# Optimization experiments

Measured on AMD Instinct MI355X. Metric: run time of the kernel, lower is better.

Reference implementation:

```python
import jax, jax.numpy as jnp
import numpy as np

V = 50000      # variables -> 2V literals
C = 200000     # clauses
E = 300000     # edges per polarity
EMB = 128
NFC = 3
ROUNDS = 26


def setup_inputs() -> dict:
    key = jax.random.key(0)
    ks = jax.random.split(key, 16)
    s = 0.05
    f32 = jnp.float32
    inp = {
        "l_pos_emb": jax.random.normal(ks[0], (V, EMB), f32) * s,
        "l_neg_emb": jax.random.normal(ks[1], (V, EMB), f32) * s,
        "c_emb": jax.random.normal(ks[2], (C, EMB), f32) * s,
        "l_mlp_W": jax.random.normal(ks[3], (NFC, EMB, EMB), f32) * s,
        "l_mlp_b": jnp.zeros((NFC, EMB), f32),
        "c_mlp_W": jax.random.normal(ks[4], (NFC, EMB, EMB), f32) * s,
        "c_mlp_b": jnp.zeros((NFC, EMB), f32),
        "l_Wih": jax.random.normal(ks[5], (4 * EMB, 2 * EMB), f32) * s,
        "l_Whh": jax.random.normal(ks[6], (4 * EMB, EMB), f32) * s,
        "l_bih": jnp.zeros((4 * EMB,), f32),
        "l_bhh": jnp.zeros((4 * EMB,), f32),
        "c_Wih": jax.random.normal(ks[7], (4 * EMB, EMB), f32) * s,
        "c_Whh": jax.random.normal(ks[8], (4 * EMB, EMB), f32) * s,
        "c_bih": jnp.zeros((4 * EMB,), f32),
        "c_bhh": jnp.zeros((4 * EMB,), f32),
        "pos_src": jax.random.randint(ks[9], (E,), 0, V, jnp.int32),
        "pos_dst": jax.random.randint(ks[10], (E,), 0, C, jnp.int32),
        "neg_src": jax.random.randint(ks[11], (E,), 0, V, jnp.int32),
        "neg_dst": jax.random.randint(ks[12], (E,), 0, C, jnp.int32),
    }
    return inp


def _mlp(x, W, b):
    # num_fc Linear layers with ReLU between (no final activation)
    n = W.shape[0]
    for i in range(n):
        x = x @ W[i] + b[i]
        if i < n - 1:
            x = jax.nn.relu(x)
    return x


def _lstm_cell(x, h, c, Wih, Whh, bih, bhh):
    # torch nn.LSTM single step; gate order i, f, g, o
    gates = x @ Wih.T + h @ Whh.T + bih + bhh
    i, f, g, o = jnp.split(gates, 4, axis=1)
    c_new = jax.nn.sigmoid(f) * c + jax.nn.sigmoid(i) * jnp.tanh(g)
    h_new = jax.nn.sigmoid(o) * jnp.tanh(c_new)
    return h_new, c_new


def reference(l_pos_emb, l_neg_emb, c_emb,
              l_mlp_W, l_mlp_b, c_mlp_W, c_mlp_b,
              l_Wih, l_Whh, l_bih, l_bhh,
              c_Wih, c_Whh, c_bih, c_bhh,
              pos_src, pos_dst, neg_src, neg_dst):
    num_v = l_pos_emb.shape[0]
    num_c = c_emb.shape[0]
    l_h = jnp.concatenate([l_pos_emb, l_neg_emb], axis=0)   # [2V, E]
    l_c = jnp.zeros_like(l_h)
    c_h = c_emb
    c_c = jnp.zeros_like(c_h)

    def round_fn(carry, _):
        l_h, l_c, c_h, c_c = carry
        # literal -> clause messages
        l_msg = _mlp(l_h, l_mlp_W, l_mlp_b)
        pos_msg, neg_msg = l_msg[:num_v], l_msg[num_v:]
        l2c = (jax.ops.segment_sum(pos_msg[pos_src], pos_dst, num_segments=num_c)
               + jax.ops.segment_sum(neg_msg[neg_src], neg_dst, num_segments=num_c))
        # clause -> literal messages (reverse edges)
        c_msg = _mlp(c_h, c_mlp_W, c_mlp_b)
        pos_c2l = jax.ops.segment_sum(c_msg[pos_dst], pos_src, num_segments=num_v)
        neg_c2l = jax.ops.segment_sum(c_msg[neg_dst], neg_src, num_segments=num_v)
        c2l = jnp.concatenate([pos_c2l, neg_c2l], axis=0)    # [2V, E]
        # flip literal hidden (pair each literal with its negation)
        flip = jnp.concatenate([l_h[num_v:], l_h[:num_v]], axis=0)
        l_x = jnp.concatenate([c2l, flip], axis=1)           # [2V, 2E]
        l_h, l_c = _lstm_cell(l_x, l_h, l_c, l_Wih, l_Whh, l_bih, l_bhh)
        c_h, c_c = _lstm_cell(l2c, c_h, c_c, c_Wih, c_Whh, c_bih, c_bhh)
        return (l_h, l_c, c_h, c_c), None

    (l_h, l_c, c_h, c_c), _ = jax.lax.scan(round_fn, (l_h, l_c, c_h, c_c),
                                           None, length=ROUNDS)
    # concat final literal and clause embeddings: [2V + C, EMB]
    return jnp.concatenate([l_h, c_h], axis=0)
```

## Files before the change

### kernel.cpp

```cpp
#include <hip/hip_runtime.h>
#include <math.h>

typedef __attribute__((ext_vector_type(8))) short short8;
typedef __attribute__((ext_vector_type(4))) float f32x4;
typedef unsigned short ushort_t;

constexpr int NV = 50000;
constexpr int NL = 100000;
constexpr int NC = 200000;
constexpr int NE = 300000;
constexpr int NROUNDS = 26;

__device__ __forceinline__ float sigf(float x) { return 1.0f / (1.0f + __expf(-x)); }

__device__ __forceinline__ void split1(float x, ushort_t* h, ushort_t* l) {
    unsigned u = __float_as_uint(x);
    *h = (ushort_t)(u >> 16);
    float lf = x - __uint_as_float(u & 0xffff0000u);
    *l = (ushort_t)(__float_as_uint(lf) >> 16);
}
__device__ __forceinline__ float recf(ushort_t h, ushort_t l) {
    return __uint_as_float((unsigned)h << 16) + __uint_as_float((unsigned)l << 16);
}

__device__ __forceinline__ void splitw(float x, ushort_t* h, ushort_t* l) {
    unsigned u = __float_as_uint(x);
    unsigned hr = (u + 0x7fffu + ((u >> 16) & 1u)) & 0xffff0000u;
    float lf = x - __uint_as_float(hr);
    unsigned ul = __float_as_uint(lf);
    *h = (ushort_t)(hr >> 16);
    *l = (ushort_t)((ul + 0x7fffu + ((ul >> 16) & 1u)) >> 16);
}


__global__ __launch_bounds__(256) void split_rows_k(
    const float* __restrict__ src, ushort_t* __restrict__ dst, int total)
{
    for (int i = blockIdx.x * 256 + threadIdx.x; i < total; i += gridDim.x * 256) {
        int row = i >> 7, c = i & 127;
        ushort_t h, l;
        split1(src[i], &h, &l);
        dst[(size_t)row * 256 + c] = h;
        dst[(size_t)row * 256 + 128 + c] = l;
    }
}

__global__ __launch_bounds__(256) void convert_out_k(
    const ushort_t* __restrict__ src, float* __restrict__ dst, int total)
{
    for (int i = blockIdx.x * 256 + threadIdx.x; i < total; i += gridDim.x * 256) {
        int row = i >> 7, c = i & 127;
        dst[i] = recf(src[(size_t)row * 256 + c], src[(size_t)row * 256 + 128 + c]);
    }
}


__global__ __launch_bounds__(256) void pack_mlp_frag(
    const float* __restrict__ W, ushort_t* __restrict__ Wh, ushort_t* __restrict__ Wl)
{
    int fid = blockIdx.x * 256 + threadIdx.x;
    if (fid >= 6144) return;
    int lane = fid & 63;
    int tile = (fid >> 6) & 7;
    int kt = (fid >> 9) & 3;
    int layer = fid >> 11;
    int l15 = lane & 15, lg = lane >> 4;
    int n = tile * 16 + l15;
#pragma unroll
    for (int j = 0; j < 8; j++) {
        int k = kt * 32 + lg * 8 + j;
        ushort_t h, l;
        splitw(W[layer * 16384 + k * 128 + n], &h, &l);
        Wh[(size_t)fid * 8 + j] = h;
        Wl[(size_t)fid * 8 + j] = l;
    }
}

__global__ __launch_bounds__(256) void pack_lstm_frag(
    const float* __restrict__ Wih, const float* __restrict__ Whh, int kih, int nstep,
    ushort_t* __restrict__ Wh, ushort_t* __restrict__ Wl)
{
    int fid = blockIdx.x * 256 + threadIdx.x;
    if (fid >= nstep * 2048) return;
    int lane = fid & 63;
    int tile = (fid >> 6) & 31;
    int kt = fid >> 11;
    int l15 = lane & 15, lg = lane >> 4;
    int n = tile * 16 + l15;
#pragma unroll
    for (int j = 0; j < 8; j++) {
        int k = kt * 32 + lg * 8 + j;
        float v = (k < kih) ? Wih[n * kih + k] : Whh[(n << 7) + (k - kih)];
        ushort_t h, l;
        splitw(v, &h, &l);
        Wh[(size_t)fid * 8 + j] = h;
        Wl[(size_t)fid * 8 + j] = l;
    }
}

__global__ __launch_bounds__(256) void csr_hist_k(
    const int* __restrict__ ps, const int* __restrict__ pd,
    const int* __restrict__ ns, const int* __restrict__ nd,
    int* __restrict__ cnt_c, int* __restrict__ cnt_l)
{
    int e = blockIdx.x * 256 + threadIdx.x;
    if (e >= NE) return;
    atomicAdd(&cnt_c[pd[e]], 1);
    atomicAdd(&cnt_c[nd[e]], 1);
    atomicAdd(&cnt_l[ps[e]], 1);
    atomicAdd(&cnt_l[NV + ns[e]], 1);
}

__global__ __launch_bounds__(256) void scan_p1(
    const int* __restrict__ cnt, int* __restrict__ partials, int n)
{
    __shared__ int sdata[256];
    int t = threadIdx.x, b = blockIdx.x;
    int base = b * 1024 + t * 4;
    int s = 0;
#pragma unroll
    for (int j = 0; j < 4; j++) { int i = base + j; if (i < n) s += cnt[i]; }
    sdata[t] = s; __syncthreads();
    for (int st = 128; st > 0; st >>= 1) {
        if (t < st) sdata[t] += sdata[t + st];
        __syncthreads();
    }
    if (t == 0) partials[b] = sdata[0];
}

__global__ __launch_bounds__(256) void scan_p2(int* __restrict__ partials, int nb, int* __restrict__ rowptr_end)
{
    __shared__ int sdata[256];
    int t = threadIdx.x;
    int v = (t < nb) ? partials[t] : 0;
    int x = v;
    sdata[t] = x; __syncthreads();
    for (int st = 1; st < 256; st <<= 1) {
        int y = (t >= st) ? sdata[t - st] : 0;
        __syncthreads();
        x += y; sdata[t] = x;
        __syncthreads();
    }
    if (t < nb) partials[t] = x - v;
    if (t == 255) *rowptr_end = sdata[255];
}

__global__ __launch_bounds__(256) void scan_p3(
    const int* __restrict__ cnt, const int* __restrict__ partials,
    int* __restrict__ rowptr, int* __restrict__ cursor, int n)
{
    __shared__ int sdata[256];
    int t = threadIdx.x, b = blockIdx.x;
    int base = b * 1024 + t * 4;
    int v[4]; int s = 0;
#pragma unroll
    for (int j = 0; j < 4; j++) { int i = base + j; v[j] = (i < n) ? cnt[i] : 0; s += v[j]; }
    int x = s;
    sdata[t] = x; __syncthreads();
    for (int st = 1; st < 256; st <<= 1) {
        int y = (t >= st) ? sdata[t - st] : 0;
        __syncthreads();
        x += y; sdata[t] = x;
        __syncthreads();
    }
    int off = partials[b] + x - s;
#pragma unroll
    for (int j = 0; j < 4; j++) {
        int i = base + j;
        if (i < n) { rowptr[i] = off; cursor[i] = off; off += v[j]; }
    }
}

__global__ __launch_bounds__(256) void csr_fill_k(
    const int* __restrict__ ps, const int* __restrict__ pd,
    const int* __restrict__ ns, const int* __restrict__ nd,
    int* __restrict__ cur_c, int* __restrict__ eidx_c,
    int* __restrict__ cur_l, int* __restrict__ eidx_l)
{
    int e = blockIdx.x * 256 + threadIdx.x;
    if (e >= NE) return;
    int p;
    p = atomicAdd(&cur_c[pd[e]], 1); eidx_c[p] = ps[e];
    p = atomicAdd(&cur_c[nd[e]], 1); eidx_c[p] = NV + ns[e];
    p = atomicAdd(&cur_l[ps[e]], 1); eidx_l[p] = pd[e];
    p = atomicAdd(&cur_l[NV + ns[e]], 1); eidx_l[p] = nd[e];
}

__global__ __launch_bounds__(256) void gather_sum_k(
    const ushort_t* __restrict__ msg, const int* __restrict__ rowptr,
    const int* __restrict__ eidx, ushort_t* __restrict__ out, int nrows)
{
    int row = (blockIdx.x * 256 + threadIdx.x) >> 6;
    if (row >= nrows) return;
    int lane = threadIdx.x & 63;
    int beg = rowptr[row], end = rowptr[row + 1];
    float a0 = 0.f, a1 = 0.f;
    for (int j = beg; j < end; j++) {
        int src = eidx[j];
        const ushort_t* p = msg + (size_t)src * 256 + lane * 2;
        unsigned hp = *reinterpret_cast<const unsigned*>(p);
        unsigned lp = *reinterpret_cast<const unsigned*>(p + 128);
        a0 += __uint_as_float(hp << 16) + __uint_as_float(lp << 16);
        a1 += __uint_as_float(hp & 0xffff0000u) + __uint_as_float(lp & 0xffff0000u);
    }
    ushort_t h0, l0, h1, l1;
    split1(a0, &h0, &l0);
    split1(a1, &h1, &l1);
    ushort_t* op = out + (size_t)row * 256 + lane * 2;
    *reinterpret_cast<unsigned*>(op) = (unsigned)h0 | ((unsigned)h1 << 16);
    *reinterpret_cast<unsigned*>(op + 128) = (unsigned)l0 | ((unsigned)l1 << 16);
}

__global__ __launch_bounds__(256, 3) void mlp3_v5(
    const ushort_t* __restrict__ x, const ushort_t* __restrict__ Wh,
    const ushort_t* __restrict__ Wl, const float* __restrict__ bias,
    ushort_t* __restrict__ y, int M)
{
    __shared__ ushort_t Xh[64][136];
    __shared__ ushort_t Xl[64][136];
    const int t = threadIdx.x;
    const int rb = blockIdx.x * 64;
    const int lane = t & 63, w = t >> 6, wr = w >> 1, wc = w & 1;
    const int l15 = lane & 15, lg = lane >> 4;

#pragma unroll
    for (int j = 0; j < 8; j++) {
        int idx = t + 256 * j;
        int plane = idx >> 10, rem = idx & 1023;
        int r = rem >> 4, c8 = (rem & 15) * 8;
        int gr = rb + r; if (gr >= M) gr = M - 1;
        uint4 v = *reinterpret_cast<const uint4*>(x + (size_t)gr * 256 + plane * 128 + c8);
        ushort_t* dst = plane ? &Xl[r][c8] : &Xh[r][c8];
        *reinterpret_cast<uint4*>(dst) = v;
    }
    __syncthreads();

    for (int layer = 0; layer < 3; layer++) {
        f32x4 acc[2][4];
#pragma unroll
        for (int m = 0; m < 2; m++)
#pragma unroll
            for (int nf = 0; nf < 4; nf++) acc[m][nf] = f32x4{0.f, 0.f, 0.f, 0.f};

        short8 bh[4], bl[4], bhn[4], bln[4];
#pragma unroll
        for (int nf = 0; nf < 4; nf++) {
            int tile = wc * 4 + nf;
            size_t off = ((size_t)((layer * 4 + 0) * 8 + tile) * 64 + lane) * 8;
            bh[nf] = *reinterpret_cast<const short8*>(Wh + off);
            bl[nf] = *reinterpret_cast<const short8*>(Wl + off);
        }

#pragma unroll
        for (int kt = 0; kt < 4; kt++) {
            short8 ah[2], al[2];
#pragma unroll
            for (int m = 0; m < 2; m++) {
                int row = wr * 32 + m * 16 + l15;
                ah[m] = *reinterpret_cast<const short8*>(&Xh[row][kt * 32 + lg * 8]);
                al[m] = *reinterpret_cast<const short8*>(&Xl[row][kt * 32 + lg * 8]);
            }
            if (kt < 3) {
#pragma unroll
                for (int nf = 0; nf < 4; nf++) {
                    int tile = wc * 4 + nf;
                    size_t off = ((size_t)((layer * 4 + kt + 1) * 8 + tile) * 64 + lane) * 8;
                    bhn[nf] = *reinterpret_cast<const short8*>(Wh + off);
                    bln[nf] = *reinterpret_cast<const short8*>(Wl + off);
                }
            }
#pragma unroll
            for (int nf = 0; nf < 4; nf++)
#pragma unroll
                for (int m = 0; m < 2; m++)
                    acc[m][nf] = __builtin_amdgcn_mfma_f32_16x16x32_bf16(ah[m], bh[nf], acc[m][nf], 0, 0, 0);
#pragma unroll
            for (int nf = 0; nf < 4; nf++)
#pragma unroll
                for (int m = 0; m < 2; m++)
                    acc[m][nf] = __builtin_amdgcn_mfma_f32_16x16x32_bf16(ah[m], bl[nf], acc[m][nf], 0, 0, 0);
#pragma unroll
            for (int nf = 0; nf < 4; nf++)
#pragma unroll
                for (int m = 0; m < 2; m++)
                    acc[m][nf] = __builtin_amdgcn_mfma_f32_16x16x32_bf16(al[m], bh[nf], acc[m][nf], 0, 0, 0);
            if (kt < 3) {
#pragma unroll
                for (int nf = 0; nf < 4; nf++) { bh[nf] = bhn[nf]; bl[nf] = bln[nf]; }
            }
        }

        float bv[4];
#pragma unroll
        for (int nf = 0; nf < 4; nf++) bv[nf] = bias[layer * 128 + wc * 64 + nf * 16 + l15];
        __syncthreads();
        if (layer < 2) {
#pragma unroll
            for (int m = 0; m < 2; m++)
#pragma unroll
                for (int nf = 0; nf < 4; nf++)
#pragma unroll
                    for (int rr = 0; rr < 4; rr++) {
                        float v = fmaxf(acc[m][nf][rr] + bv[nf], 0.f);
                        ushort_t h, l;
                        split1(v, &h, &l);
                        int rw = wr * 32 + m * 16 + lg * 4 + rr;
                        int cl = wc * 64 + nf * 16 + l15;
                        Xh[rw][cl] = h;
                        Xl[rw][cl] = l;
                    }
            __syncthreads();
        } else {
#pragma unroll
            for (int m = 0; m < 2; m++)
#pragma unroll
                for (int rr = 0; rr < 4; rr++) {
                    int gr = rb + wr * 32 + m * 16 + lg * 4 + rr;
                    if (gr < M) {
#pragma unroll
                        for (int nf = 0; nf < 4; nf++) {
                            float v = acc[m][nf][rr] + bv[nf];
                            ushort_t h, l;
                            split1(v, &h, &l);
                            size_t p = (size_t)gr * 256 + wc * 64 + nf * 16 + l15;
                            y[p] = h;
                            y[p + 128] = l;
                        }
                    }
                }
        }
    }
}

template <int NKT, bool FLIP>
__global__ __launch_bounds__(256, 2) void lstm_v6(
    const ushort_t* __restrict__ A0, const ushort_t* __restrict__ A1, const ushort_t* __restrict__ A2,
    const ushort_t* __restrict__ Bh_g, const ushort_t* __restrict__ Bl_g,
    const float* __restrict__ bih, const float* __restrict__ bhh,
    float* __restrict__ c_st, ushort_t* __restrict__ h_out, int M)
{
    __shared__ uint4 As[2][1024];
    __shared__ uint4 Bs[2][1024];
    const int t = threadIdx.x;
    const int s = blockIdx.x;
    const int rb = blockIdx.y * 128;
    const int lane = t & 63, w = t >> 6, wr = w >> 1, wc = w & 1;
    const int l15 = lane & 15, lg = lane >> 4;

    f32x4 acc[4][4];
#pragma unroll
    for (int m = 0; m < 4; m++)
#pragma unroll
        for (int g = 0; g < 4; g++) acc[m][g] = f32x4{0.f, 0.f, 0.f, 0.f};

#pragma unroll
    for (int i = 0; i < 4; i++) {
        int idx = t + 256 * i;
        int plane = idx >> 9, rem = idx & 511;
        int tile = rem >> 6, ln = rem & 63;
        int gr = rb + tile * 16 + (ln & 15); if (gr >= M) gr = M - 1;
        As[0][idx] = *reinterpret_cast<const uint4*>(
            A0 + (size_t)gr * 256 + plane * 128 + (ln >> 4) * 8);
    }
#pragma unroll
    for (int i = 0; i < 4; i++) {
        int idx = t + 256 * i;
        int f = idx >> 6, ln = idx & 63;
        int sel = f >> 3, ft = f & 7;
        int gt = (ft >> 1) * 8 + s * 2 + (ft & 1);
        const ushort_t* bsrc = sel ? Bl_g : Bh_g;
        Bs[0][idx] = *reinterpret_cast<const uint4*>(bsrc + ((size_t)gt * 64 + ln) * 8);
    }
    __syncthreads();

    int cur = 0;
#pragma unroll
    for (int kt = 0; kt < NKT; kt++) {
        uint4 a_stg[4], b_stg[4];
        if (kt + 1 < NKT) {
            const int kn = kt + 1;
            const int seg = kn >> 2;
            const ushort_t* src = (seg == 0) ? A0 : ((seg == 1) ? A1 : A2);
            const bool useF = FLIP && (seg == 1);
            const int kco = (kn & 3) * 32;
#pragma unroll
            for (int i = 0; i < 4; i++) {
                int idx = t + 256 * i;
                int plane = idx >> 9, rem = idx & 511;
                int tile = rem >> 6, ln = rem & 63;
                int gr = rb + tile * 16 + (ln & 15); if (gr >= M) gr = M - 1;
                if (useF) gr = (gr < NV) ? gr + NV : gr - NV;
                a_stg[i] = *reinterpret_cast<const uint4*>(
                    src + (size_t)gr * 256 + plane * 128 + kco + (ln >> 4) * 8);
            }
#pragma unroll
            for (int i = 0; i < 4; i++) {
                int idx = t + 256 * i;
                int f = idx >> 6, ln = idx & 63;
                int sel = f >> 3, ft = f & 7;
                int gt = (ft >> 1) * 8 + s * 2 + (ft & 1);
                const ushort_t* bsrc = sel ? Bl_g : Bh_g;
                b_stg[i] = *reinterpret_cast<const uint4*>(bsrc + ((size_t)(kn * 32 + gt) * 64 + ln) * 8);
            }
        }

        const uint4* Ab = As[cur];
        const uint4* Bb = Bs[cur];
        short8 ah[4], al[4];
#pragma unroll
        for (int m = 0; m < 4; m++) {
            int tile = wr * 4 + m;
            ah[m] = *reinterpret_cast<const short8*>(&Ab[tile * 64 + lane]);
            al[m] = *reinterpret_cast<const short8*>(&Ab[512 + tile * 64 + lane]);
        }
#pragma unroll
        for (int g = 0; g < 4; g++) {
            short8 bh = *reinterpret_cast<const short8*>(&Bb[(g * 2 + wc) * 64 + lane]);
            short8 bl = *reinterpret_cast<const short8*>(&Bb[(8 + g * 2 + wc) * 64 + lane]);
#pragma unroll
            for (int m = 0; m < 4; m++)
                acc[m][g] = __builtin_amdgcn_mfma_f32_16x16x32_bf16(ah[m], bh, acc[m][g], 0, 0, 0);
#pragma unroll
            for (int m = 0; m < 4; m++)
                acc[m][g] = __builtin_amdgcn_mfma_f32_16x16x32_bf16(ah[m], bl, acc[m][g], 0, 0, 0);
#pragma unroll
            for (int m = 0; m < 4; m++)
                acc[m][g] = __builtin_amdgcn_mfma_f32_16x16x32_bf16(al[m], bh, acc[m][g], 0, 0, 0);
        }

        if (kt + 1 < NKT) {
            int nb = cur ^ 1;
#pragma unroll
            for (int i = 0; i < 4; i++) As[nb][t + 256 * i] = a_stg[i];
#pragma unroll
            for (int i = 0; i < 4; i++) Bs[nb][t + 256 * i] = b_stg[i];
        }
        __syncthreads();
        cur ^= 1;
    }

    const int colc = s * 32 + wc * 16 + l15;
    float bs4[4];
#pragma unroll
    for (int g = 0; g < 4; g++) bs4[g] = bih[g * 128 + colc] + bhh[g * 128 + colc];
#pragma unroll
    for (int m = 0; m < 4; m++)
#pragma unroll
        for (int rr = 0; rr < 4; rr++) {
            int gr = rb + wr * 64 + m * 16 + lg * 4 + rr;
            if (gr >= M) continue;
            float gi = acc[m][0][rr] + bs4[0];
            float gf = acc[m][1][rr] + bs4[1];
            float gg = acc[m][2][rr] + bs4[2];
            float go = acc[m][3][rr] + bs4[3];
            size_t pc = (size_t)gr * 128 + colc;
            float cold = c_st[pc];
            float cn = sigf(gf) * cold + sigf(gi) * tanhf(gg);
            float hn = sigf(go) * tanhf(cn);
            c_st[pc] = cn;
            ushort_t hh, hl;
            split1(hn, &hh, &hl);
            size_t ph = (size_t)gr * 256 + colc;
            h_out[ph] = hh;
            h_out[ph + 128] = hl;
        }
}

extern "C" void kernel_launch(void* const* d_in, const int* in_sizes, int n_in,
                              void* d_out, int out_size, void* d_ws, size_t ws_size,
                              hipStream_t stream)
{
    const float* l_pos   = (const float*)d_in[0];
    const float* l_neg   = (const float*)d_in[1];
    const float* c_emb   = (const float*)d_in[2];
    const float* l_mlp_W = (const float*)d_in[3];
    const float* l_mlp_b = (const float*)d_in[4];
    const float* c_mlp_W = (const float*)d_in[5];
    const float* c_mlp_b = (const float*)d_in[6];
    const float* l_Wih   = (const float*)d_in[7];
    const float* l_Whh   = (const float*)d_in[8];
    const float* l_bih   = (const float*)d_in[9];
    const float* l_bhh   = (const float*)d_in[10];
    const float* c_Wih   = (const float*)d_in[11];
    const float* c_Whh   = (const float*)d_in[12];
    const float* c_bih   = (const float*)d_in[13];
    const float* c_bhh   = (const float*)d_in[14];
    const int* pos_src   = (const int*)d_in[15];
    const int* pos_dst   = (const int*)d_in[16];
    const int* neg_src   = (const int*)d_in[17];
    const int* neg_dst   = (const int*)d_in[18];

    float* out = (float*)d_out;
    ushort_t* l_hQ = (ushort_t*)d_out;
    ushort_t* c_hQ = (ushort_t*)(out + (size_t)NL * 128);

    float* wsp = (float*)d_ws;
    ushort_t* l_hP  = (ushort_t*)wsp; wsp += (size_t)NL * 128;
    float*    l_c   = wsp;            wsp += (size_t)NL * 128;
    float*    c_c   = wsp;            wsp += (size_t)NC * 128;
    ushort_t* l_msg = (ushort_t*)wsp; wsp += (size_t)NL * 128;
    ushort_t* c_hP  = (ushort_t*)wsp; wsp += (size_t)NC * 128;
    ushort_t* l2c   = (ushort_t*)wsp; wsp += (size_t)NC * 128;
    ushort_t* c2l = l_msg;

    ushort_t* us = (ushort_t*)wsp;
    ushort_t* mlpLh = us; us += 3 * 128 * 128;
    ushort_t* mlpLl = us; us += 3 * 128 * 128;
    ushort_t* mlpCh = us; us += 3 * 128 * 128;
    ushort_t* mlpCl = us; us += 3 * 128 * 128;
    ushort_t* lstmLh = us; us += 512 * 384;
    ushort_t* lstmLl = us; us += 512 * 384;
    ushort_t* lstmCh = us; us += 512 * 256;
    ushort_t* lstmCl = us; us += 512 * 256;

    int* ip = (int*)us;
    int* cnt_c    = ip; ip += NC;
    int* rowptr_c = ip; ip += NC + 1;
    int* cur_c    = ip; ip += NC;
    int* eidx_c   = ip; ip += 2 * NE;
    int* cnt_l    = ip; ip += NL;
    int* rowptr_l = ip; ip += NL + 1;
    int* cur_l    = ip; ip += NL;
    int* eidx_l   = ip; ip += 2 * NE;
    int* part_c   = ip; ip += 256;
    int* part_l   = ip; ip += 256;

    split_rows_k<<<2048, 256, 0, stream>>>(l_pos, l_hP, NV * 128);
    split_rows_k<<<2048, 256, 0, stream>>>(l_neg, l_hP + (size_t)NV * 256, NV * 128);
    split_rows_k<<<2048, 256, 0, stream>>>(c_emb, c_hP, NC * 128);
    hipMemsetAsync(l_c, 0, (size_t)NL * 128 * 4, stream);
    hipMemsetAsync(c_c, 0, (size_t)NC * 128 * 4, stream);

    pack_mlp_frag<<<24, 256, 0, stream>>>(l_mlp_W, mlpLh, mlpLl);
    pack_mlp_frag<<<24, 256, 0, stream>>>(c_mlp_W, mlpCh, mlpCl);
    pack_lstm_frag<<<96, 256, 0, stream>>>(l_Wih, l_Whh, 256, 12, lstmLh, lstmLl);
    pack_lstm_frag<<<64, 256, 0, stream>>>(c_Wih, c_Whh, 128, 8, lstmCh, lstmCl);

    hipMemsetAsync(cnt_c, 0, NC * sizeof(int), stream);
    hipMemsetAsync(cnt_l, 0, NL * sizeof(int), stream);
    constexpr int EB = (NE + 255) / 256;
    csr_hist_k<<<EB, 256, 0, stream>>>(pos_src, pos_dst, neg_src, neg_dst, cnt_c, cnt_l);
    constexpr int NBC = (NC + 1023) / 1024;
    constexpr int NBL = (NL + 1023) / 1024;
    scan_p1<<<NBC, 256, 0, stream>>>(cnt_c, part_c, NC);
    scan_p2<<<1, 256, 0, stream>>>(part_c, NBC, rowptr_c + NC);
    scan_p3<<<NBC, 256, 0, stream>>>(cnt_c, part_c, rowptr_c, cur_c, NC);
    scan_p1<<<NBL, 256, 0, stream>>>(cnt_l, part_l, NL);
    scan_p2<<<1, 256, 0, stream>>>(part_l, NBL, rowptr_l + NL);
    scan_p3<<<NBL, 256, 0, stream>>>(cnt_l, part_l, rowptr_l, cur_l, NL);
    csr_fill_k<<<EB, 256, 0, stream>>>(pos_src, pos_dst, neg_src, neg_dst,
                                       cur_c, eidx_c, cur_l, eidx_l);

    ushort_t* l_cur = l_hP;
    ushort_t* l_nxt = l_hQ;
    ushort_t* c_cur = c_hP;
    ushort_t* c_oth = c_hQ;

    for (int r = 0; r < NROUNDS; r++) {
        mlp3_v5<<<(NL + 63) / 64, 256, 0, stream>>>(l_cur, mlpLh, mlpLl, l_mlp_b, l_msg, NL);
        mlp3_v5<<<(NC + 63) / 64, 256, 0, stream>>>(c_cur, mlpCh, mlpCl, c_mlp_b, c_oth, NC);

        gather_sum_k<<<NC * 64 / 256, 256, 0, stream>>>(l_msg, rowptr_c, eidx_c, l2c, NC);
        gather_sum_k<<<NL * 64 / 256, 256, 0, stream>>>(c_oth, rowptr_l, eidx_l, c2l, NL);

        lstm_v6<12, true><<<dim3(4, (NL + 127) / 128), 256, 0, stream>>>(
            c2l, l_cur, l_cur, lstmLh, lstmLl, l_bih, l_bhh, l_c, l_nxt, NL);
        lstm_v6<8, false><<<dim3(4, (NC + 127) / 128), 256, 0, stream>>>(
            l2c, c_cur, nullptr, lstmCh, lstmCl, c_bih, c_bhh, c_c, c_oth, NC);

        ushort_t* t2 = l_cur; l_cur = l_nxt; l_nxt = t2;
        t2 = c_cur; c_cur = c_oth; c_oth = t2;
    }
    convert_out_k<<<2048, 256, 0, stream>>>(l_hP, out, NL * 128);
    convert_out_k<<<2048, 256, 0, stream>>>(c_hP, out + (size_t)NL * 128, NC * 128);
    (void)in_sizes; (void)n_in; (void)out_size; (void)ws_size;
}
```

Before: 23.15 ms.

## Read LSTM weight fragments from global memory, drop B LDS staging, remap blocks

The LSTM kernel stops staging weight fragments in shared memory and loads the B fragments straight from global memory (expected to hit in L2) inside the MFMA loop. This halves LDS use, so occupancy is raised to 3 blocks per CU. The grid becomes 1D with a swizzle that groups 8 row tiles for each of the 4 column slices, to improve L2 reuse of the A rows across slices. The trade-off is that global-load latency now sits directly before the MFMAs, with no prefetch of B.

```diff
diff --git a/kernel.cpp b/kernel.cpp
--- a/kernel.cpp
+++ b/kernel.cpp
@@ -333,17 +333,21 @@
 }
 
 template <int NKT, bool FLIP>
-__global__ __launch_bounds__(256, 2) void lstm_v6(
+__global__ __launch_bounds__(256, 3) void lstm_v7(
     const ushort_t* __restrict__ A0, const ushort_t* __restrict__ A1, const ushort_t* __restrict__ A2,
     const ushort_t* __restrict__ Bh_g, const ushort_t* __restrict__ Bl_g,
     const float* __restrict__ bih, const float* __restrict__ bhh,
     float* __restrict__ c_st, ushort_t* __restrict__ h_out, int M)
 {
     __shared__ uint4 As[2][1024];
-    __shared__ uint4 Bs[2][1024];
+    const int wg = blockIdx.x;
+    const int r8 = wg & 7, j = wg >> 3;
+    const int s = j & 3;
+    const int tile_id = r8 + 8 * (j >> 2);
+    const int rb = tile_id * 128;
+    if (rb >= M) return;
+
     const int t = threadIdx.x;
-    const int s = blockIdx.x;
-    const int rb = blockIdx.y * 128;
     const int lane = t & 63, w = t >> 6, wr = w >> 1, wc = w & 1;
     const int l15 = lane & 15, lg = lane >> 4;
 
@@ -357,26 +361,17 @@
     for (int i = 0; i < 4; i++) {
         int idx = t + 256 * i;
         int plane = idx >> 9, rem = idx & 511;
-        int tile = rem >> 6, ln = rem & 63;
-        int gr = rb + tile * 16 + (ln & 15); if (gr >= M) gr = M - 1;
+        int tl = rem >> 6, ln = rem & 63;
+        int gr = rb + tl * 16 + (ln & 15); if (gr >= M) gr = M - 1;
         As[0][idx] = *reinterpret_cast<const uint4*>(
             A0 + (size_t)gr * 256 + plane * 128 + (ln >> 4) * 8);
     }
-#pragma unroll
-    for (int i = 0; i < 4; i++) {
-        int idx = t + 256 * i;
-        int f = idx >> 6, ln = idx & 63;
-        int sel = f >> 3, ft = f & 7;
-        int gt = (ft >> 1) * 8 + s * 2 + (ft & 1);
-        const ushort_t* bsrc = sel ? Bl_g : Bh_g;
-        Bs[0][idx] = *reinterpret_cast<const uint4*>(bsrc + ((size_t)gt * 64 + ln) * 8);
-    }
     __syncthreads();
 
     int cur = 0;
 #pragma unroll
     for (int kt = 0; kt < NKT; kt++) {
-        uint4 a_stg[4], b_stg[4];
+        uint4 a_stg[4];
         if (kt + 1 < NKT) {
             const int kn = kt + 1;
             const int seg = kn >> 2;
@@ -387,36 +382,28 @@
             for (int i = 0; i < 4; i++) {
                 int idx = t + 256 * i;
                 int plane = idx >> 9, rem = idx & 511;
-                int tile = rem >> 6, ln = rem & 63;
-                int gr = rb + tile * 16 + (ln & 15); if (gr >= M) gr = M - 1;
+                int tl = rem >> 6, ln = rem & 63;
+                int gr = rb + tl * 16 + (ln & 15); if (gr >= M) gr = M - 1;
                 if (useF) gr = (gr < NV) ? gr + NV : gr - NV;
                 a_stg[i] = *reinterpret_cast<const uint4*>(
                     src + (size_t)gr * 256 + plane * 128 + kco + (ln >> 4) * 8);
             }
-#pragma unroll
-            for (int i = 0; i < 4; i++) {
-                int idx = t + 256 * i;
-                int f = idx >> 6, ln = idx & 63;
-                int sel = f >> 3, ft = f & 7;
-                int gt = (ft >> 1) * 8 + s * 2 + (ft & 1);
-                const ushort_t* bsrc = sel ? Bl_g : Bh_g;
-                b_stg[i] = *reinterpret_cast<const uint4*>(bsrc + ((size_t)(kn * 32 + gt) * 64 + ln) * 8);
-            }
         }
 
         const uint4* Ab = As[cur];
-        const uint4* Bb = Bs[cur];
         short8 ah[4], al[4];
 #pragma unroll
         for (int m = 0; m < 4; m++) {
-            int tile = wr * 4 + m;
-            ah[m] = *reinterpret_cast<const short8*>(&Ab[tile * 64 + lane]);
-            al[m] = *reinterpret_cast<const short8*>(&Ab[512 + tile * 64 + lane]);
+            int tl = wr * 4 + m;
+            ah[m] = *reinterpret_cast<const short8*>(&Ab[tl * 64 + lane]);
+            al[m] = *reinterpret_cast<const short8*>(&Ab[512 + tl * 64 + lane]);
         }
 #pragma unroll
         for (int g = 0; g < 4; g++) {
-            short8 bh = *reinterpret_cast<const short8*>(&Bb[(g * 2 + wc) * 64 + lane]);
-            short8 bl = *reinterpret_cast<const short8*>(&Bb[(8 + g * 2 + wc) * 64 + lane]);
+            int gt = g * 8 + s * 2 + wc;
+            size_t off = ((size_t)(kt * 32 + gt) * 64 + lane) * 8;
+            short8 bh = *reinterpret_cast<const short8*>(Bh_g + off);
+            short8 bl = *reinterpret_cast<const short8*>(Bl_g + off);
 #pragma unroll
             for (int m = 0; m < 4; m++)
                 acc[m][g] = __builtin_amdgcn_mfma_f32_16x16x32_bf16(ah[m], bh, acc[m][g], 0, 0, 0);
@@ -432,8 +419,6 @@
             int nb = cur ^ 1;
 #pragma unroll
             for (int i = 0; i < 4; i++) As[nb][t + 256 * i] = a_stg[i];
-#pragma unroll
-            for (int i = 0; i < 4; i++) Bs[nb][t + 256 * i] = b_stg[i];
         }
         __syncthreads();
         cur ^= 1;
@@ -551,6 +536,9 @@
     csr_fill_k<<<EB, 256, 0, stream>>>(pos_src, pos_dst, neg_src, neg_dst,
                                        cur_c, eidx_c, cur_l, eidx_l);
 
+    constexpr int TL = (NL + 127) / 128, TLP = ((TL + 7) / 8) * 8;
+    constexpr int TC = (NC + 127) / 128, TCP = ((TC + 7) / 8) * 8;
+
     ushort_t* l_cur = l_hP;
     ushort_t* l_nxt = l_hQ;
     ushort_t* c_cur = c_hP;
@@ -563,9 +551,9 @@
         gather_sum_k<<<NC * 64 / 256, 256, 0, stream>>>(l_msg, rowptr_c, eidx_c, l2c, NC);
         gather_sum_k<<<NL * 64 / 256, 256, 0, stream>>>(c_oth, rowptr_l, eidx_l, c2l, NL);
 
-        lstm_v6<12, true><<<dim3(4, (NL + 127) / 128), 256, 0, stream>>>(
+        lstm_v7<12, true><<<4 * TLP, 256, 0, stream>>>(
             c2l, l_cur, l_cur, lstmLh, lstmLl, l_bih, l_bhh, l_c, l_nxt, NL);
-        lstm_v6<8, false><<<dim3(4, (NC + 127) / 128), 256, 0, stream>>>(
+        lstm_v7<8, false><<<4 * TCP, 256, 0, stream>>>(
             l2c, c_cur, nullptr, lstmCh, lstmCl, c_bih, c_bhh, c_c, c_oth, NC);
 
         ushort_t* t2 = l_cur; l_cur = l_nxt; l_nxt = t2;
```

Result: faster. 22.19 ms (-4.2%).
